# Performance work log

Hardware: AMD Instinct MI355X
Metric: run time of the kernel (lower is better)

Reference implementation:

```python
import jax, jax.numpy as jnp
import numpy as np

DIM = 768
NUM_HEADS = 12
HEAD_DIM = DIM // NUM_HEADS


def setup_inputs() -> dict:
    key = jax.random.key(0)
    k0, k1, k2 = jax.random.split(key, 3)
    B, N = 8, 1024
    x = jax.random.normal(k0, (B, N, DIM), dtype=jnp.float32)
    w_qkv = jax.random.normal(k1, (DIM, 3 * DIM), dtype=jnp.float32) * (DIM ** -0.5)
    b_qkv = jnp.zeros((3 * DIM,), dtype=jnp.float32)
    w_proj = jax.random.normal(k2, (DIM, DIM), dtype=jnp.float32) * (DIM ** -0.5)
    b_proj = jnp.zeros((DIM,), dtype=jnp.float32)
    return {"x": x, "w_qkv": w_qkv, "b_qkv": b_qkv, "w_proj": w_proj, "b_proj": b_proj}


def reference(x, w_qkv, b_qkv, w_proj, b_proj):
    B, N, C = x.shape
    scale = HEAD_DIM ** -0.5
    qkv = x @ w_qkv + b_qkv                                  # [B, N, 3*C]
    qkv = qkv.reshape(B, N, 3, NUM_HEADS, HEAD_DIM).transpose(2, 0, 3, 1, 4)
    q, k, v = qkv[0], qkv[1], qkv[2]                          # each [B, H, N, hd]
    attn = jnp.einsum('bhqd,bhkd->bhqk', q, k) * scale        # [B, H, N, N]
    attn = jax.nn.softmax(attn, axis=-1)
    out = jnp.einsum('bhqk,bhkd->bhqd', attn, v)              # [B, H, N, hd]
    out = out.transpose(0, 2, 1, 3).reshape(B, N, C)
    return out @ w_proj + b_proj
```

## Files before the change

### kernel.cpp

```cpp
#include <hip/hip_runtime.h>
#include <cstdint>
#include <cmath>

#define B_ 8
#define S_ 1024
#define D_ 768
#define H_ 12
#define HD_ 64

typedef __bf16 bf16;
typedef __attribute__((ext_vector_type(8))) __bf16 bf16x8;
typedef __attribute__((ext_vector_type(4))) float floatx4;

typedef const __attribute__((address_space(1))) unsigned int* gas_ptr;
typedef __attribute__((address_space(3))) unsigned int* las_ptr;

__device__ __forceinline__ void async_ld16(const void* g, void* l) {
    gas_ptr gp = (gas_ptr)(uintptr_t)g;
    las_ptr lp = (las_ptr)(unsigned)(uintptr_t)l;
    __builtin_amdgcn_global_load_lds(gp, lp, 16, 0, 0);
}

__device__ __forceinline__ void xcd_swizzle(int& bx, int& by) {
    const int nx = gridDim.x, ny = gridDim.y;
    const int lin = blockIdx.y * nx + blockIdx.x;
    const int xcd = lin & 7;
    const int loc = lin >> 3;
    by = xcd * (ny >> 3) + loc / nx;
    bx = loc % nx;
}

__device__ __forceinline__ void stage32(const bf16* __restrict__ A,
                                        const bf16* __restrict__ Bt,
                                        long m0, long n0, long K, int kb,
                                        bf16* Asb, bf16* Bsb, int tid) {
#pragma unroll
    for (int r = 0; r < 2; r++) {
        const int idx = r * 256 + tid;
        const int rr  = idx >> 2;
        const int kc  = (idx & 3) * 8;
        async_ld16(A  + (m0 + rr) * K + kb + kc, (char*)Asb + idx * 16);
        async_ld16(Bt + (n0 + rr) * K + kb + kc, (char*)Bsb + idx * 16);
    }
}

__device__ __forceinline__ void transpose_dev(const float* __restrict__ in,
                                              bf16* __restrict__ out,
                                              int N, int K, int n0, int k0,
                                              bf16 (*tile)[66], int tid) {
#pragma unroll
    for (int r = 0; r < 4; r++) {
        int idx = r * 256 + tid;
        int row = idx >> 4;
        int c0  = (idx & 15) * 4;
        float4 v = *(const float4*)(in + (size_t)(k0 + row) * N + n0 + c0);
        tile[c0 + 0][row] = (bf16)v.x;
        tile[c0 + 1][row] = (bf16)v.y;
        tile[c0 + 2][row] = (bf16)v.z;
        tile[c0 + 3][row] = (bf16)v.w;
    }
    __syncthreads();
#pragma unroll
    for (int r = 0; r < 2; r++) {
        int idx = r * 256 + tid;
        int orow = idx >> 3;
        int kk   = (idx & 7) * 8;
        union { bf16x8 v; bf16 e[8]; } u;
#pragma unroll
        for (int j = 0; j < 8; j++) u.e[j] = tile[orow][kk + j];
        *(bf16x8*)(out + (size_t)(n0 + orow) * K + k0 + kk) = u.v;
    }
}

__global__ __launch_bounds__(256) void prep_all(
    const float* __restrict__ x, const float* __restrict__ w_qkv,
    const float* __restrict__ w_proj,
    bf16* __restrict__ xb, bf16* __restrict__ wqkvt, bf16* __restrict__ wprojt)
{
    __shared__ bf16 tile[64][66];
    const int blk = blockIdx.x, tid = threadIdx.x;
    if (blk < 6144) {
        int i = (blk * 256 + tid) * 4;
        float4 v = *(const float4*)(x + i);
        xb[i]     = (bf16)v.x;
        xb[i + 1] = (bf16)v.y;
        xb[i + 2] = (bf16)v.z;
        xb[i + 3] = (bf16)v.w;
    } else if (blk < 6576) {
        int t = blk - 6144;
        transpose_dev(w_qkv, wqkvt, 2304, 768, (t % 36) * 64, (t / 36) * 64, tile, tid);
    } else {
        int t = blk - 6576;
        transpose_dev(w_proj, wprojt, 768, 768, (t % 12) * 64, (t / 12) * 64, tile, tid);
    }
}

__global__ void transpose_v(const bf16* __restrict__ vbuf, bf16* __restrict__ vt) {
    __shared__ bf16 tile[64][66];
    const int tid = threadIdx.x;
    const int kt = blockIdx.x, h = blockIdx.y, b = blockIdx.z;
    const bf16* src = vbuf + ((size_t)b * S_ + (size_t)kt * 64) * D_ + h * 64;
#pragma unroll
    for (int r = 0; r < 2; r++) {
        int idx = r * 256 + tid;
        int kr = idx >> 3;
        int d0 = (idx & 7) * 8;
        bf16x8 v = *(const bf16x8*)(src + (size_t)kr * D_ + d0);
#pragma unroll
        for (int j = 0; j < 8; j++) {
            int p  = d0 + j;
            int dt = (p >> 2) + 16 * (p & 3);
            tile[dt][kr] = v[j];
        }
    }
    __syncthreads();
    bf16* dst = vt + ((size_t)(b * H_ + h) * 64) * 1024 + kt * 64;
#pragma unroll
    for (int r = 0; r < 2; r++) {
        int idx = r * 256 + tid;
        int dr = idx >> 3;
        int k0 = (idx & 7) * 8;
        union { bf16x8 v; bf16 e[8]; } u;
#pragma unroll
        for (int j = 0; j < 8; j++) {
            int kp  = k0 + j;
            int grp = kp & 32;
            int w32 = kp & 31;
            int gg  = w32 >> 3;
            int jj  = w32 & 7;
            int tk  = grp + ((jj < 4) ? (4 * gg + jj) : (16 + 4 * gg + jj - 4));
            u.e[j] = tile[dr][tk];
        }
        *(bf16x8*)(dst + (size_t)dr * 1024 + k0) = u.v;
    }
}

__global__ __launch_bounds__(256, 2) void gemm_qkv(
    const bf16* __restrict__ A, const bf16* __restrict__ Bt,
    const float* __restrict__ bias,
    bf16* __restrict__ qpack, bf16* __restrict__ kpack, bf16* __restrict__ vbuf)
{
    __shared__ __align__(16) bf16 As[4][128 * 32];
    __shared__ __align__(16) bf16 Bs[4][128 * 32];
    const int N = 2304, K = 768;
    const int NKT = K / 32;

    const int tid  = threadIdx.x;
    const int lane = tid & 63;
    const int w    = tid >> 6;
    const int wm   = (w >> 1) * 64;
    const int wn   = (w & 1) * 64;
    int bx, by;
    xcd_swizzle(bx, by);
    const long m0  = (long)by * 128;
    const long n0  = (long)bx * 128;
    const int c    = lane & 15;
    const int g    = lane >> 4;

    const floatx4 fzero = {0.f, 0.f, 0.f, 0.f};
    floatx4 acc[4][4];
#pragma unroll
    for (int i = 0; i < 4; i++)
#pragma unroll
        for (int j = 0; j < 4; j++) acc[i][j] = fzero;

    stage32(A, Bt, m0, n0, K, 0,  As[0], Bs[0], tid);
    stage32(A, Bt, m0, n0, K, 32, As[1], Bs[1], tid);

    for (int kt = 0; kt < NKT; kt++) {
        const int cb = kt & 3;
        if (kt + 2 < NKT) {
            stage32(A, Bt, m0, n0, K, (kt + 2) * 32, As[(kt + 2) & 3], Bs[(kt + 2) & 3], tid);
            asm volatile("s_waitcnt vmcnt(8)" ::: "memory");
        } else if (kt + 1 < NKT) {
            asm volatile("s_waitcnt vmcnt(4)" ::: "memory");
        } else {
            asm volatile("s_waitcnt vmcnt(0)" ::: "memory");
        }
        __builtin_amdgcn_s_barrier();

        bf16x8 af[4], bfr[4];
#pragma unroll
        for (int i = 0; i < 4; i++) {
            af[i]  = *(const bf16x8*)(As[cb] + (wm + i * 16 + c) * 32 + g * 8);
            bfr[i] = *(const bf16x8*)(Bs[cb] + (wn + i * 16 + c) * 32 + g * 8);
        }
#pragma unroll
        for (int i = 0; i < 4; i++)
#pragma unroll
            for (int j = 0; j < 4; j++)
                acc[i][j] = __builtin_amdgcn_mfma_f32_16x16x32_bf16(af[i], bfr[j], acc[i][j], 0, 0, 0);
    }

    const int head = (int)((n0 + wn) >> 6);
    const int rm   = wm + g * 4;
    float bv[4];
#pragma unroll
    for (int j = 0; j < 4; j++) bv[j] = bias[(int)n0 + wn + c + 16 * j];
    const int bb    = (int)(m0 >> 10);
    const int sbase = ((int)m0 & 1023) + rm;

    if (head < 24) {
        const float sc = (head < 12) ? 0.125f : 1.0f;
        bf16* dst = ((head < 12) ? qpack : kpack)
                  + (((size_t)((bb * H_ + (head < 12 ? head : head - 12)) * 1024 + sbase)) << 6)
                  + 4 * c;
#pragma unroll
        for (int i = 0; i < 4; i++)
#pragma unroll
            for (int e = 0; e < 4; e++) {
                union { bf16 h4[4]; uint64_t u; } pk;
#pragma unroll
                for (int j = 0; j < 4; j++) pk.h4[j] = (bf16)((acc[i][j][e] + bv[j]) * sc);
                *(uint64_t*)(dst + (size_t)(i * 16 + e) * 64) = pk.u;
            }
    } else {
        bf16* dst = vbuf + ((size_t)(bb * 1024 + sbase)) * 768 + (head - 24) * 64 + 4 * c;
#pragma unroll
        for (int i = 0; i < 4; i++)
#pragma unroll
            for (int e = 0; e < 4; e++) {
                union { bf16 h4[4]; uint64_t u; } pk;
#pragma unroll
                for (int j = 0; j < 4; j++) pk.h4[j] = (bf16)(acc[i][j][e] + bv[j]);
                *(uint64_t*)(dst + (size_t)(i * 16 + e) * 768) = pk.u;
            }
    }
}

__global__ __launch_bounds__(256, 2) void gemm_bt(
    const bf16* __restrict__ A, const bf16* __restrict__ Bt,
    const float* __restrict__ bias, float* __restrict__ C,
    int M, int N, int K)
{
    __shared__ __align__(16) bf16 As[4][128 * 32];
    __shared__ __align__(16) bf16 Bs[4][128 * 32];

    const int tid  = threadIdx.x;
    const int lane = tid & 63;
    const int w    = tid >> 6;
    const int wm   = (w >> 1) * 64;
    const int wn   = (w & 1) * 64;
    int bx, by;
    xcd_swizzle(bx, by);
    const long m0  = (long)by * 128;
    const long n0  = (long)bx * 128;
    const int c    = lane & 15;
    const int g    = lane >> 4;
    const int NKT  = K / 32;

    const floatx4 fzero = {0.f, 0.f, 0.f, 0.f};
    floatx4 acc[4][4];
#pragma unroll
    for (int i = 0; i < 4; i++)
#pragma unroll
        for (int j = 0; j < 4; j++) acc[i][j] = fzero;

    stage32(A, Bt, m0, n0, K, 0,  As[0], Bs[0], tid);
    stage32(A, Bt, m0, n0, K, 32, As[1], Bs[1], tid);

    for (int kt = 0; kt < NKT; kt++) {
        const int cb = kt & 3;
        if (kt + 2 < NKT) {
            stage32(A, Bt, m0, n0, K, (kt + 2) * 32, As[(kt + 2) & 3], Bs[(kt + 2) & 3], tid);
            asm volatile("s_waitcnt vmcnt(8)" ::: "memory");
        } else if (kt + 1 < NKT) {
            asm volatile("s_waitcnt vmcnt(4)" ::: "memory");
        } else {
            asm volatile("s_waitcnt vmcnt(0)" ::: "memory");
        }
        __builtin_amdgcn_s_barrier();

        bf16x8 af[4], bfr[4];
#pragma unroll
        for (int i = 0; i < 4; i++) {
            af[i]  = *(const bf16x8*)(As[cb] + (wm + i * 16 + c) * 32 + g * 8);
            bfr[i] = *(const bf16x8*)(Bs[cb] + (wn + i * 16 + c) * 32 + g * 8);
        }
#pragma unroll
        for (int i = 0; i < 4; i++)
#pragma unroll
            for (int j = 0; j < 4; j++)
                acc[i][j] = __builtin_amdgcn_mfma_f32_16x16x32_bf16(af[i], bfr[j], acc[i][j], 0, 0, 0);
    }

    const int cn = wn + c;
    const int rm = wm + g * 4;
#pragma unroll
    for (int j = 0; j < 4; j++) {
        const long gn = n0 + cn + j * 16;
        const float bv = bias[gn];
#pragma unroll
        for (int i = 0; i < 4; i++) {
            const long gm = m0 + rm + i * 16;
#pragma unroll
            for (int e = 0; e < 4; e++)
                C[(gm + e) * (long)N + gn] = acc[i][j][e] + bv;
        }
    }
}

__device__ __forceinline__ void attn_stage(const bf16* __restrict__ kpb,
                                           const bf16* __restrict__ vtb,
                                           int kg, bf16* Kb, bf16* Vb, int tid) {
    const int dc = tid >> 7, key = (tid >> 2) & 31, dch = tid & 3;
    async_ld16(kpb + (size_t)(kg + key) * 64 + dc * 32 + dch * 8, (char*)Kb + tid * 16);
    const int d = tid >> 2, kch = tid & 3;
    async_ld16(vtb + (size_t)d * 1024 + kg + kch * 8, (char*)Vb + tid * 16);
}

__global__ __launch_bounds__(256, 3) void attn_fused(
    const bf16* __restrict__ qpack, const bf16* __restrict__ kpack,
    const bf16* __restrict__ vt, bf16* __restrict__ outp)
{
    __shared__ __align__(16) bf16 Ks[4][2048];
    __shared__ __align__(16) bf16 Vs[4][2048];

    const int tid  = threadIdx.x;
    const int lane = tid & 63;
    const int w    = tid >> 6;
    const int g    = lane >> 4;
    const int c    = lane & 15;

    const int id = blockIdx.x;
    const int bh = id % 96;
    const int qt = id / 96;
    const int h  = bh >> 3;
    const int b  = bh & 7;
    const int q0 = qt * 128 + w * 32;
    const bf16* qpb = qpack + ((size_t)(b * H_ + h) * 1024) * 64;
    const bf16* kpb = kpack + ((size_t)(b * H_ + h) * 1024) * 64;
    const bf16* vtb = vt    + ((size_t)(b * H_ + h) * 64) * 1024;

    bf16x8 qf[2][2];
#pragma unroll
    for (int qb = 0; qb < 2; qb++)
#pragma unroll
        for (int dc = 0; dc < 2; dc++)
            qf[qb][dc] = *(const bf16x8*)(qpb + (size_t)(q0 + qb * 16 + c) * 64 + dc * 32 + g * 8);

    union { uint32_t u[4]; bf16x8 v; } onesu;
    onesu.u[0] = onesu.u[1] = onesu.u[2] = onesu.u[3] = 0x3F803F80u;
    const bf16x8 onesf = onesu.v;

    const floatx4 fzero = {0.f, 0.f, 0.f, 0.f};
    floatx4 oacc[2][4];
    floatx4 lacc[2];
#pragma unroll
    for (int qb = 0; qb < 2; qb++) {
        lacc[qb] = fzero;
#pragma unroll
        for (int db = 0; db < 4; db++) oacc[qb][db] = fzero;
    }

    attn_stage(kpb, vtb, 0,  Ks[0], Vs[0], tid);
    attn_stage(kpb, vtb, 32, Ks[1], Vs[1], tid);

    for (int kt = 0; kt < 32; kt++) {
        const int cb = kt & 3;
        if (kt + 2 < 32) {
            attn_stage(kpb, vtb, (kt + 2) * 32, Ks[(kt + 2) & 3], Vs[(kt + 2) & 3], tid);
            asm volatile("s_waitcnt vmcnt(4)" ::: "memory");
        } else if (kt + 1 < 32) {
            asm volatile("s_waitcnt vmcnt(2)" ::: "memory");
        } else {
            asm volatile("s_waitcnt vmcnt(0)" ::: "memory");
        }
        __builtin_amdgcn_s_barrier();

        bf16x8 kf[2][2];
#pragma unroll
        for (int kb = 0; kb < 2; kb++)
#pragma unroll
            for (int dc = 0; dc < 2; dc++)
                kf[kb][dc] = *(const bf16x8*)(Ks[cb] + (dc * 32 + kb * 16 + c) * 32 + g * 8);

        bf16x8 vf[4];
#pragma unroll
        for (int db = 0; db < 4; db++)
            vf[db] = *(const bf16x8*)(Vs[cb] + (db * 16 + c) * 32 + g * 8);

#pragma unroll
        for (int qb = 0; qb < 2; qb++) {
            floatx4 s0 = fzero, s1 = fzero;
#pragma unroll
            for (int dc = 0; dc < 2; dc++) {
                s0 = __builtin_amdgcn_mfma_f32_16x16x32_bf16(kf[0][dc], qf[qb][dc], s0, 0, 0, 0);
                s1 = __builtin_amdgcn_mfma_f32_16x16x32_bf16(kf[1][dc], qf[qb][dc], s1, 0, 0, 0);
            }
            union { bf16 e[8]; bf16x8 v; } pa;
#pragma unroll
            for (int e4 = 0; e4 < 4; e4++) {
                pa.e[e4]     = (bf16)__expf(s0[e4]);
                pa.e[e4 + 4] = (bf16)__expf(s1[e4]);
            }
            lacc[qb] = __builtin_amdgcn_mfma_f32_16x16x32_bf16(onesf, pa.v, lacc[qb], 0, 0, 0);
#pragma unroll
            for (int db = 0; db < 4; db++)
                oacc[qb][db] = __builtin_amdgcn_mfma_f32_16x16x32_bf16(vf[db], pa.v, oacc[qb][db], 0, 0, 0);
        }
    }

#pragma unroll
    for (int qb = 0; qb < 2; qb++) {
        const float linv = 1.0f / lacc[qb][0];
        bf16* orow = outp + ((size_t)b * S_ + q0 + qb * 16 + c) * D_ + h * 64;
#pragma unroll
        for (int db = 0; db < 4; db++)
#pragma unroll
            for (int f = 0; f < 2; f++) {
                union { bf16 hh[2]; uint32_t u; } pk_;
                pk_.hh[0] = (bf16)(oacc[qb][db][2 * f]     * linv);
                pk_.hh[1] = (bf16)(oacc[qb][db][2 * f + 1] * linv);
                *(uint32_t*)(orow + db * 16 + 4 * g + 2 * f) = pk_.u;
            }
    }
}

extern "C" void kernel_launch(void* const* d_in, const int* in_sizes, int n_in,
                              void* d_out, int out_size, void* d_ws, size_t ws_size,
                              hipStream_t stream) {
    const float* x      = (const float*)d_in[0];
    const float* w_qkv  = (const float*)d_in[1];
    const float* b_qkv  = (const float*)d_in[2];
    const float* w_proj = (const float*)d_in[3];
    const float* b_proj = (const float*)d_in[4];
    float* out = (float*)d_out;

    bf16* xb     = (bf16*)d_ws;
    bf16* wqkvt  = xb     + (size_t)8192 * 768;
    bf16* wprojt = wqkvt  + (size_t)2304 * 768;
    bf16* qpack  = wprojt + (size_t)768 * 768;
    bf16* kpack  = qpack  + (size_t)96 * 1024 * 64;
    bf16* vbuf   = kpack  + (size_t)96 * 1024 * 64;
    bf16* vt     = vbuf   + (size_t)8192 * 768;
    bf16* attnb  = xb;

    prep_all<<<6720, 256, 0, stream>>>(x, w_qkv, w_proj, xb, wqkvt, wprojt);
    gemm_qkv<<<dim3(18, 64), 256, 0, stream>>>(xb, wqkvt, b_qkv, qpack, kpack, vbuf);
    transpose_v<<<dim3(16, 12, 8), 256, 0, stream>>>(vbuf, vt);
    attn_fused<<<768, 256, 0, stream>>>(qpack, kpack, vt, attnb);
    gemm_bt<<<dim3(6, 64), 256, 0, stream>>>(attnb, wprojt, b_proj, out, 8192, 768, 768);
}
```

Before: 181.5 us.

## Enlarge GEMM block tile to 256x128 with triple-buffered LDS pipeline

Both the QKV and output-projection GEMMs move from a 128x128 to a 256x128 block tile, with each wave computing a 128x64 sub-tile (8x4 MFMA accumulators). The shared-memory ring drops from four stages to three, and a second barrier is added after the MFMAs so a buffer is not overwritten while another wave still reads it. The intent is more reuse of each B fragment and less global and LDS traffic per FLOP. In exchange, each wave holds twice as many accumulator registers, and the grids halve (576 and 192 blocks), which may underfill the 256 CUs, especially for the projection GEMM.

New measurement: 184.8 us. Within noise of the previous version (+1.8%).

```diff
diff --git a/kernel.cpp b/kernel.cpp
--- a/kernel.cpp
+++ b/kernel.cpp
@@ -30,17 +30,19 @@
     bx = loc % nx;
 }
 
-__device__ __forceinline__ void stage32(const bf16* __restrict__ A,
-                                        const bf16* __restrict__ Bt,
-                                        long m0, long n0, long K, int kb,
-                                        bf16* Asb, bf16* Bsb, int tid) {
+__device__ __forceinline__ void stage_ab(const bf16* __restrict__ A,
+                                         const bf16* __restrict__ Bt,
+                                         long m0, long n0, long K, int kb,
+                                         bf16* Asb, bf16* Bsb, int tid) {
+#pragma unroll
+    for (int r = 0; r < 4; r++) {
+        const int idx = r * 256 + tid;
+        async_ld16(A + (m0 + (idx >> 2)) * K + kb + (idx & 3) * 8, (char*)Asb + idx * 16);
+    }
 #pragma unroll
     for (int r = 0; r < 2; r++) {
         const int idx = r * 256 + tid;
-        const int rr  = idx >> 2;
-        const int kc  = (idx & 3) * 8;
-        async_ld16(A  + (m0 + rr) * K + kb + kc, (char*)Asb + idx * 16);
-        async_ld16(Bt + (n0 + rr) * K + kb + kc, (char*)Bsb + idx * 16);
+        async_ld16(Bt + (n0 + (idx >> 2)) * K + kb + (idx & 3) * 8, (char*)Bsb + idx * 16);
     }
 }
 
@@ -140,56 +142,59 @@
     const float* __restrict__ bias,
     bf16* __restrict__ qpack, bf16* __restrict__ kpack, bf16* __restrict__ vbuf)
 {
-    __shared__ __align__(16) bf16 As[4][128 * 32];
-    __shared__ __align__(16) bf16 Bs[4][128 * 32];
+    __shared__ __align__(16) bf16 As[3][256 * 32];
+    __shared__ __align__(16) bf16 Bs[3][128 * 32];
     const int N = 2304, K = 768;
-    const int NKT = K / 32;
+    const int NKT = 24;
 
     const int tid  = threadIdx.x;
     const int lane = tid & 63;
     const int w    = tid >> 6;
-    const int wm   = (w >> 1) * 64;
+    const int wm   = (w >> 1) * 128;
     const int wn   = (w & 1) * 64;
     int bx, by;
     xcd_swizzle(bx, by);
-    const long m0  = (long)by * 128;
+    const long m0  = (long)by * 256;
     const long n0  = (long)bx * 128;
     const int c    = lane & 15;
     const int g    = lane >> 4;
 
     const floatx4 fzero = {0.f, 0.f, 0.f, 0.f};
-    floatx4 acc[4][4];
-#pragma unroll
-    for (int i = 0; i < 4; i++)
+    floatx4 acc[8][4];
+#pragma unroll
+    for (int i = 0; i < 8; i++)
 #pragma unroll
         for (int j = 0; j < 4; j++) acc[i][j] = fzero;
 
-    stage32(A, Bt, m0, n0, K, 0,  As[0], Bs[0], tid);
-    stage32(A, Bt, m0, n0, K, 32, As[1], Bs[1], tid);
+    stage_ab(A, Bt, m0, n0, K, 0,  As[0], Bs[0], tid);
+    stage_ab(A, Bt, m0, n0, K, 32, As[1], Bs[1], tid);
 
     for (int kt = 0; kt < NKT; kt++) {
-        const int cb = kt & 3;
+        const int cb = kt % 3;
         if (kt + 2 < NKT) {
-            stage32(A, Bt, m0, n0, K, (kt + 2) * 32, As[(kt + 2) & 3], Bs[(kt + 2) & 3], tid);
-            asm volatile("s_waitcnt vmcnt(8)" ::: "memory");
+            stage_ab(A, Bt, m0, n0, K, (kt + 2) * 32, As[(kt + 2) % 3], Bs[(kt + 2) % 3], tid);
+            asm volatile("s_waitcnt vmcnt(12)" ::: "memory");
         } else if (kt + 1 < NKT) {
-            asm volatile("s_waitcnt vmcnt(4)" ::: "memory");
+            asm volatile("s_waitcnt vmcnt(6)" ::: "memory");
         } else {
             asm volatile("s_waitcnt vmcnt(0)" ::: "memory");
         }
         __builtin_amdgcn_s_barrier();
 
-        bf16x8 af[4], bfr[4];
-#pragma unroll
-        for (int i = 0; i < 4; i++) {
+        bf16x8 af[8], bfr[4];
+#pragma unroll
+        for (int i = 0; i < 8; i++)
             af[i]  = *(const bf16x8*)(As[cb] + (wm + i * 16 + c) * 32 + g * 8);
-            bfr[i] = *(const bf16x8*)(Bs[cb] + (wn + i * 16 + c) * 32 + g * 8);
-        }
-#pragma unroll
-        for (int i = 0; i < 4; i++)
+#pragma unroll
+        for (int j = 0; j < 4; j++)
+            bfr[j] = *(const bf16x8*)(Bs[cb] + (wn + j * 16 + c) * 32 + g * 8);
+#pragma unroll
+        for (int i = 0; i < 8; i++)
 #pragma unroll
             for (int j = 0; j < 4; j++)
                 acc[i][j] = __builtin_amdgcn_mfma_f32_16x16x32_bf16(af[i], bfr[j], acc[i][j], 0, 0, 0);
+
+        __builtin_amdgcn_s_barrier();
     }
 
     const int head = (int)((n0 + wn) >> 6);
@@ -206,7 +211,7 @@
                   + (((size_t)((bb * H_ + (head < 12 ? head : head - 12)) * 1024 + sbase)) << 6)
                   + 4 * c;
 #pragma unroll
-        for (int i = 0; i < 4; i++)
+        for (int i = 0; i < 8; i++)
 #pragma unroll
             for (int e = 0; e < 4; e++) {
                 union { bf16 h4[4]; uint64_t u; } pk;
@@ -217,7 +222,7 @@
     } else {
         bf16* dst = vbuf + ((size_t)(bb * 1024 + sbase)) * 768 + (head - 24) * 64 + 4 * c;
 #pragma unroll
-        for (int i = 0; i < 4; i++)
+        for (int i = 0; i < 8; i++)
 #pragma unroll
             for (int e = 0; e < 4; e++) {
                 union { bf16 h4[4]; uint64_t u; } pk;
@@ -233,55 +238,58 @@
     const float* __restrict__ bias, float* __restrict__ C,
     int M, int N, int K)
 {
-    __shared__ __align__(16) bf16 As[4][128 * 32];
-    __shared__ __align__(16) bf16 Bs[4][128 * 32];
+    __shared__ __align__(16) bf16 As[3][256 * 32];
+    __shared__ __align__(16) bf16 Bs[3][128 * 32];
 
     const int tid  = threadIdx.x;
     const int lane = tid & 63;
     const int w    = tid >> 6;
-    const int wm   = (w >> 1) * 64;
+    const int wm   = (w >> 1) * 128;
     const int wn   = (w & 1) * 64;
     int bx, by;
     xcd_swizzle(bx, by);
-    const long m0  = (long)by * 128;
+    const long m0  = (long)by * 256;
     const long n0  = (long)bx * 128;
     const int c    = lane & 15;
     const int g    = lane >> 4;
     const int NKT  = K / 32;
 
     const floatx4 fzero = {0.f, 0.f, 0.f, 0.f};
-    floatx4 acc[4][4];
-#pragma unroll
-    for (int i = 0; i < 4; i++)
+    floatx4 acc[8][4];
+#pragma unroll
+    for (int i = 0; i < 8; i++)
 #pragma unroll
         for (int j = 0; j < 4; j++) acc[i][j] = fzero;
 
-    stage32(A, Bt, m0, n0, K, 0,  As[0], Bs[0], tid);
-    stage32(A, Bt, m0, n0, K, 32, As[1], Bs[1], tid);
+    stage_ab(A, Bt, m0, n0, K, 0,  As[0], Bs[0], tid);
+    stage_ab(A, Bt, m0, n0, K, 32, As[1], Bs[1], tid);
 
     for (int kt = 0; kt < NKT; kt++) {
-        const int cb = kt & 3;
+        const int cb = kt % 3;
         if (kt + 2 < NKT) {
-            stage32(A, Bt, m0, n0, K, (kt + 2) * 32, As[(kt + 2) & 3], Bs[(kt + 2) & 3], tid);
-            asm volatile("s_waitcnt vmcnt(8)" ::: "memory");
+            stage_ab(A, Bt, m0, n0, K, (kt + 2) * 32, As[(kt + 2) % 3], Bs[(kt + 2) % 3], tid);
+            asm volatile("s_waitcnt vmcnt(12)" ::: "memory");
         } else if (kt + 1 < NKT) {
-            asm volatile("s_waitcnt vmcnt(4)" ::: "memory");
+            asm volatile("s_waitcnt vmcnt(6)" ::: "memory");
         } else {
             asm volatile("s_waitcnt vmcnt(0)" ::: "memory");
         }
         __builtin_amdgcn_s_barrier();
 
-        bf16x8 af[4], bfr[4];
-#pragma unroll
-        for (int i = 0; i < 4; i++) {
+        bf16x8 af[8], bfr[4];
+#pragma unroll
+        for (int i = 0; i < 8; i++)
             af[i]  = *(const bf16x8*)(As[cb] + (wm + i * 16 + c) * 32 + g * 8);
-            bfr[i] = *(const bf16x8*)(Bs[cb] + (wn + i * 16 + c) * 32 + g * 8);
-        }
-#pragma unroll
-        for (int i = 0; i < 4; i++)
+#pragma unroll
+        for (int j = 0; j < 4; j++)
+            bfr[j] = *(const bf16x8*)(Bs[cb] + (wn + j * 16 + c) * 32 + g * 8);
+#pragma unroll
+        for (int i = 0; i < 8; i++)
 #pragma unroll
             for (int j = 0; j < 4; j++)
                 acc[i][j] = __builtin_amdgcn_mfma_f32_16x16x32_bf16(af[i], bfr[j], acc[i][j], 0, 0, 0);
+
+        __builtin_amdgcn_s_barrier();
     }
 
     const int cn = wn + c;
@@ -291,7 +299,7 @@
         const long gn = n0 + cn + j * 16;
         const float bv = bias[gn];
 #pragma unroll
-        for (int i = 0; i < 4; i++) {
+        for (int i = 0; i < 8; i++) {
             const long gm = m0 + rm + i * 16;
 #pragma unroll
             for (int e = 0; e < 4; e++)
@@ -437,8 +445,8 @@
     bf16* attnb  = xb;
 
     prep_all<<<6720, 256, 0, stream>>>(x, w_qkv, w_proj, xb, wqkvt, wprojt);
-    gemm_qkv<<<dim3(18, 64), 256, 0, stream>>>(xb, wqkvt, b_qkv, qpack, kpack, vbuf);
+    gemm_qkv<<<dim3(18, 32), 256, 0, stream>>>(xb, wqkvt, b_qkv, qpack, kpack, vbuf);
     transpose_v<<<dim3(16, 12, 8), 256, 0, stream>>>(vbuf, vt);
     attn_fused<<<768, 256, 0, stream>>>(qpack, kpack, vt, attnb);
-    gemm_bt<<<dim3(6, 64), 256, 0, stream>>>(attnb, wprojt, b_proj, out, 8192, 768, 768);
-}
+    gemm_bt<<<dim3(6, 32), 256, 0, stream>>>(attnb, wprojt, b_proj, out, 8192, 768, 768);
+}
```
